# Performance work log

Hardware: AMD Instinct MI355X
Metric: run time of the kernel (lower is better)

The kernel has to match this reference:

```python
import jax, jax.numpy as jnp
import numpy as np

N_WORDS = 4096
N_HEADS = 512
EMB = 768          # input_size
HID = 1024         # hidden_size
DIST = 64          # dist_emb_size (forced by Conv1d(64, ...))
SENT_LEN = 64      # fixed sentence length -> static max padded length
PAIR_F = 2 * EMB + DIST  # 1600


def setup_inputs() -> dict:
    key = jax.random.key(0)
    ks = jax.random.split(key, 14)
    words = jax.random.normal(ks[0], (N_WORDS, EMB), dtype=jnp.float32)
    heads_ids = jax.random.randint(ks[1], (N_HEADS,), 0, N_WORDS, dtype=jnp.int64)
    sent_id = (jnp.arange(N_WORDS) // SENT_LEN).astype(jnp.int32)  # sorted, contiguous sentences
    s = 0.02
    return {
        "words": words,
        "heads_ids": heads_ids,
        "sent_id": sent_id,
        "emb_table": jax.random.normal(ks[2], (128, DIST), dtype=jnp.float32) * s,
        "W1": jax.random.normal(ks[3], (PAIR_F, HID), dtype=jnp.float32) * s,
        "b1": jnp.zeros((HID,), jnp.float32),
        "W2": jax.random.normal(ks[4], (HID, 256), dtype=jnp.float32) * s,
        "b2": jnp.zeros((256,), jnp.float32),
        "W3": jax.random.normal(ks[5], (256, DIST), dtype=jnp.float32) * s,
        "b3": jnp.zeros((DIST,), jnp.float32),
        "cw1": jax.random.normal(ks[6], (4, DIST, 3), dtype=jnp.float32) * s,  # Conv1d(64,4,3,1,1)
        "cb1": jnp.zeros((4,), jnp.float32),
        "cw2": jax.random.normal(ks[7], (2, 4, 3), dtype=jnp.float32) * s,    # Conv1d(4,2,3,1,1)
        "cb2": jnp.zeros((2,), jnp.float32),
    }


def _conv1d(x, w, b):
    # x: [N, C_in, L], w: [C_out, C_in, 3], padding=1, stride=1 (torch Conv1d semantics)
    y = jax.lax.conv_general_dilated(x, w, window_strides=(1,), padding=((1, 1),),
                                     dimension_numbers=("NCH", "OIH", "NCH"))
    return y + b[None, :, None]


def reference(words, heads_ids, sent_id, emb_table, W1, b1, W2, b2, W3, b3, cw1, cb1, cw2, cb2):
    n_words = words.shape[0]
    heads = heads_ids.astype(jnp.int32)
    H = heads.shape[0]

    # relative positions & distance-embedding ids, clamped to bucket 127 outside [-63, 63]
    rel = heads[:, None] - jnp.arange(n_words, dtype=jnp.int32)[None, :]      # [H, W]
    eid = rel + 63
    eid = jnp.where((eid < 0) | (eid > 126), 127, eid)

    # per-head sentence span (sent_id is sorted & contiguous)
    sh = sent_id[heads]
    starts = jnp.searchsorted(sent_id, sh, side="left")
    lengths = jnp.searchsorted(sent_id, sh, side="right") - starts            # [H]

    # padded ragged layout: row i holds words of head i's sentence, left-packed
    j = jnp.arange(SENT_LEN, dtype=jnp.int32)
    cols = starts[:, None] + j[None, :]                                       # [H, L]
    mask = j[None, :] < lengths[:, None]                                      # [H, L]
    cols_c = jnp.clip(cols, 0, n_words - 1)

    head_w = words[heads]                                                     # [H, E]
    col_w = words[cols_c]                                                     # [H, L, E]
    dist = emb_table[jnp.take_along_axis(eid, cols_c, axis=1)]                # [H, L, DIST]
    feat = jnp.concatenate(
        [jnp.broadcast_to(head_w[:, None, :], col_w.shape), col_w, dist], axis=-1)
    feat = jnp.where(mask[..., None], feat, jnp.zeros((), feat.dtype))        # zero padding rows (as torch)

    # FFNN (dropout is identity in eval mode)
    x = jax.nn.relu(feat @ W1 + b1)
    x = jax.nn.relu(x @ W2 + b2)
    x = x @ W3 + b3                                                           # [H, L, 64]

    # conv stack over the padded ragged axis
    x = _conv1d(x.transpose(0, 2, 1), cw1, cb1)
    x = _conv1d(x, cw2, cb2)
    res = x.transpose(0, 2, 1)                                                # [H, L, 2]

    # scatter back into [H, n_words, 2]; masked slots get out-of-range col -> dropped
    rows = jnp.broadcast_to(jnp.arange(H, dtype=jnp.int32)[:, None], mask.shape)
    cols_sc = jnp.where(mask, cols, n_words)
    scores = jnp.full((H, n_words, 2), -jnp.inf, dtype=words.dtype)
    scores = scores.at[rows, cols_sc].set(res, mode="drop")

    # eval-mode validity log-mask
    valid_starts = jnp.log((rel >= 0).astype(words.dtype))
    valid_ends = jnp.log((rel <= 0).astype(words.dtype))
    valid = jnp.stack([valid_starts, valid_ends], axis=2)
    return scores + valid
```

## Files before the change

kernel.cpp:

```cpp
#include <hip/hip_runtime.h>
#include <math.h>

#define NW   4096
#define NH   512
#define EMBD 768
#define HIDD 1024
#define DISTD 64
#define SLEN 64

#define NEG_BIG (-1.0e30f)

typedef __attribute__((ext_vector_type(8))) short short8;
typedef __attribute__((ext_vector_type(16))) float f32x16;
typedef __attribute__((ext_vector_type(4))) float f32x4;

#define MFMA32(a, b, c) __builtin_amdgcn_mfma_f32_32x32x16_bf16((a), (b), (c), 0, 0, 0)
#define MFMA16(a, b, c) __builtin_amdgcn_mfma_f32_16x16x32_bf16((a), (b), (c), 0, 0, 0)

__device__ __forceinline__ unsigned short f2bf(float f) {
    unsigned u = __float_as_uint(f);
    u += 0x7FFFu + ((u >> 16) & 1u);
    return (unsigned short)(u >> 16);
}
__device__ __forceinline__ float bf2f(unsigned short s) {
    return __uint_as_float(((unsigned)s) << 16);
}
__device__ __forceinline__ unsigned cvtpk(float lo, float hi) {
    unsigned r;
    asm("v_cvt_pk_bf16_f32 %0, %1, %2" : "=v"(r) : "v"(lo), "v"(hi));
    return r;
}
__device__ __forceinline__ short8 pack8(float f0, float f1, float f2, float f3,
                                        float f4, float f5, float f6, float f7) {
    union { unsigned u[4]; short8 s; } r;
    r.u[0] = cvtpk(f0, f1); r.u[1] = cvtpk(f2, f3);
    r.u[2] = cvtpk(f4, f5); r.u[3] = cvtpk(f6, f7);
    return r.s;
}

__device__ __forceinline__ void pack_b32_dev(long t, const float* __restrict__ src,
                                             int ld, int nb32, int KB,
                                             unsigned short* __restrict__ dst)
{
    int l = (int)(t & 63); long u = t >> 6;
    int nb = (int)(u % nb32); int kb = (int)(u / nb32);
    int row0 = kb * 16 + ((l >> 5) << 3);
    int col  = (nb << 5) + (l & 31);
    const float* s = src + (size_t)row0 * ld + col;
    short8 v;
#pragma unroll
    for (int j = 0; j < 8; ++j) v[j] = (short)f2bf(s[(size_t)j * ld]);
    *(short8*)(dst + (((size_t)nb * KB + kb) << 9) + l * 8) = v;
}

__device__ __forceinline__ void pack_b16_dev(long t, const float* __restrict__ src,
                                             int ld, int nb16, int KB,
                                             unsigned short* __restrict__ dst)
{
    int l = (int)(t & 63); long u = t >> 6;
    int nb = (int)(u % nb16); int kb = (int)(u / nb16);
    int row0 = kb * 32 + ((l >> 4) << 3);
    int col  = (nb << 4) + (l & 15);
    const float* s = src + (size_t)row0 * ld + col;
    short8 v;
#pragma unroll
    for (int j = 0; j < 8; ++j) v[j] = (short)f2bf(s[(size_t)j * ld]);
    *(short8*)(dst + (((size_t)nb * KB + kb) << 9) + l * 8) = v;
}

__device__ __forceinline__ void cvt8_dev(long i, const float* __restrict__ src,
                                         unsigned short* __restrict__ dst)
{
    const float* s = src + i * 8;
    short8 v;
#pragma unroll
    for (int j = 0; j < 8; ++j) v[j] = (short)f2bf(s[j]);
    *(short8*)(dst + i * 8) = v;
}

__global__ __launch_bounds__(256)
void prep_kernel(const float* __restrict__ words, const float* __restrict__ emb,
                 const float* __restrict__ W1, const float* __restrict__ W2,
                 const float* __restrict__ W3,
                 const int* __restrict__ heads, const int* __restrict__ sent_id,
                 unsigned short* __restrict__ wordsb, unsigned short* __restrict__ wpack,
                 unsigned short* __restrict__ embb,
                 unsigned short* __restrict__ W1pa, unsigned short* __restrict__ W1px,
                 unsigned short* __restrict__ W1pd,
                 unsigned short* __restrict__ W2p, unsigned short* __restrict__ W3p,
                 int* __restrict__ starts, int* __restrict__ lens)
{
    const int b = blockIdx.x, tid = threadIdx.x;
    if (b < 1536) {
        cvt8_dev((long)b * 256 + tid, words, wordsb);
    } else if (b < 3072) {
        long t = (long)(b - 1536) * 256 + tid;
        int r = (int)(t / 96), g = (int)(t % 96);
        const float* s = words + (size_t)r * EMBD + g * 8;
        short8 v;
#pragma unroll
        for (int j = 0; j < 8; ++j) v[j] = (short)f2bf(s[j]);
        int m = r >> 5, kb = g >> 1, lane = (r & 31) + 32 * (g & 1);
        *(short8*)(wpack + (((size_t)m * 48 + kb) << 9) + lane * 8) = v;
    } else if (b < 3076) {
        cvt8_dev((long)(b - 3072) * 256 + tid, emb, embb);
    } else if (b < 3460) {
        pack_b32_dev((long)(b - 3076) * 256 + tid, W1, HIDD, 32, 48, W1pa);
    } else if (b < 3844) {
        pack_b32_dev((long)(b - 3460) * 256 + tid, W1 + (size_t)768 * HIDD, HIDD, 32, 48, W1px);
    } else if (b < 3876) {
        pack_b32_dev((long)(b - 3844) * 256 + tid, W1 + (size_t)1536 * HIDD, HIDD, 32, 4, W1pd);
    } else if (b < 4004) {
        pack_b32_dev((long)(b - 3876) * 256 + tid, W2, 256, 8, 64, W2p);
    } else if (b < 4012) {
        pack_b16_dev((long)(b - 4004) * 256 + tid, W3, 64, 4, 8, W3p);
    } else {
        int h = (b - 4012) * 256 + tid;
        if (h < NH) {
            int head = heads[h];
            int s = sent_id[head];
            int lo = 0, hi = NW;
            while (lo < hi) { int mid = (lo + hi) >> 1; if (sent_id[mid] < s) lo = mid + 1; else hi = mid; }
            int start = lo;
            lo = 0; hi = NW;
            while (lo < hi) { int mid = (lo + hi) >> 1; if (sent_id[mid] <= s) lo = mid + 1; else hi = mid; }
            int len = lo - start;
            if (len > SLEN) len = SLEN;
            starts[h] = start;
            lens[h] = len;
        }
    }
}

__global__ __launch_bounds__(256, 4)
void gemms_kernel(const unsigned short* __restrict__ wordsb,
                  const unsigned short* __restrict__ wpack,
                  const unsigned short* __restrict__ embb,
                  const unsigned short* __restrict__ W1pa,
                  const unsigned short* __restrict__ W1px,
                  const unsigned short* __restrict__ W1pd,
                  const float* __restrict__ b1, const int* __restrict__ heads,
                  unsigned short* __restrict__ XwP, unsigned short* __restrict__ Hcb,
                  unsigned short* __restrict__ Dtb)
{
    const int b = blockIdx.x, tid = threadIdx.x;
    const int l = tid & 63, w = tid >> 6;

    if (b < 1024) {
        const int mB = b >> 3, nB = b & 7;
        const int cbg = nB * 4 + w;
        const unsigned short* ap = wpack + (((size_t)mB * 48) << 9) + l * 8;
        const unsigned short* bp = W1px + (((size_t)cbg * 48) << 9) + l * 8;
        f32x16 acc = {};
#pragma unroll
        for (int kk = 0; kk < 48; ++kk) {
            short8 a = *(const short8*)(ap + ((size_t)kk << 9));
            short8 bb = *(const short8*)(bp + ((size_t)kk << 9));
            acc = MFMA32(a, bb, acc);
        }
        const int col = cbg * 32 + (l & 31);
        const float bv = b1[col];
        const int kb2 = 2 * cbg + ((l & 31) >> 4);
        const int j = l & 7;
        const int lhalf = 32 * ((l >> 3) & 1);
        unsigned short* cp = XwP + (((size_t)mB * 64 + kb2) << 9) + j;
#pragma unroll
        for (int r = 0; r < 16; ++r) {
            int rr = (r & 3) + 8 * (r >> 2) + 4 * (l >> 5);
            cp[(rr + lhalf) * 8] = f2bf(acc[r] + bv);
        }
    } else if (b < 1152) {
        const int q = b - 1024;
        const int mB = q >> 3, nB = q & 7;
        const int cbg = nB * 4 + w;
        int row = heads[mB * 32 + (l & 31)];
        const unsigned short* ap = wordsb + (size_t)row * EMBD + ((l >> 5) << 3);
        const unsigned short* bp = W1pa + (((size_t)cbg * 48) << 9) + l * 8;
        f32x16 acc = {};
#pragma unroll
        for (int kk = 0; kk < 48; ++kk) {
            short8 a = *(const short8*)(ap + kk * 16);
            short8 bb = *(const short8*)(bp + ((size_t)kk << 9));
            acc = MFMA32(a, bb, acc);
        }
        const int col = cbg * 32 + (l & 31);
#pragma unroll
        for (int r = 0; r < 16; ++r) {
            int rr = mB * 32 + (r & 3) + 8 * (r >> 2) + 4 * (l >> 5);
            Hcb[(size_t)rr * HIDD + col] = f2bf(acc[r]);
        }
    } else {
        const int q = b - 1152;
        const int mB = q >> 3, nB = q & 7;
        const int cbg = nB * 4 + w;
        const unsigned short* ap = embb + (size_t)(mB * 32 + (l & 31)) * DISTD + ((l >> 5) << 3);
        const unsigned short* bp = W1pd + (((size_t)cbg * 4) << 9) + l * 8;
        f32x16 acc = {};
#pragma unroll
        for (int kk = 0; kk < 4; ++kk) {
            short8 a = *(const short8*)(ap + kk * 16);
            short8 bb = *(const short8*)(bp + ((size_t)kk << 9));
            acc = MFMA32(a, bb, acc);
        }
        const int col = cbg * 32 + (l & 31);
#pragma unroll
        for (int r = 0; r < 16; ++r) {
            int rr = mB * 32 + (r & 3) + 8 * (r >> 2) + 4 * (l >> 5);
            Dtb[(size_t)rr * HIDD + col] = f2bf(acc[r]);
        }
    }
}

__global__ __launch_bounds__(256)
void packd_kernel(const unsigned short* __restrict__ Dtb,
                  unsigned short* __restrict__ PDr)
{
    const int tid = threadIdx.x, l = tid & 63;
    const int c = blockIdx.x * 4 + (tid >> 6);
    const int s = c / 192, rem = c % 192;
    const int m = rem >> 6, kb = rem & 63;
    const int row = 126 - (s + 32 * m + (l & 31));
    const int koff = kb * 16 + ((l >> 5) << 3);
    short8 v = *(const short8*)(Dtb + (size_t)row * HIDD + koff);
    *(short8*)(PDr + ((size_t)c << 9) + l * 8) = v;
}

#define NT 32
__global__ __launch_bounds__(512)
void head_kernel(const unsigned short* __restrict__ XwP,
                 const unsigned short* __restrict__ Hcb,
                 const unsigned short* __restrict__ PDr,
                 const unsigned short* __restrict__ W2p,
                 const float* __restrict__ b2,
                 const unsigned short* __restrict__ W3p,
                 const float* __restrict__ b3,
                 const float* __restrict__ cw1, const float* __restrict__ cb1,
                 const float* __restrict__ cw2, const float* __restrict__ cb2,
                 const int* __restrict__ heads, const int* __restrict__ starts,
                 const int* __restrict__ lens,
                 float* __restrict__ out)
{
    __shared__ char smem[67584];
    unsigned short* Ast = (unsigned short*)smem;
    unsigned short* Bst = (unsigned short*)(smem + 16384);
    unsigned short* x2s = (unsigned short*)smem;
    float* x3s = (float*)smem;
    float* y1s = (float*)(smem + 35328);
    float* y2s = (float*)(smem + 37376);

    const int tid = threadIdx.x;
    const int l = tid & 63, w = tid >> 6;
    const int h0 = blockIdx.x * 2;

    const int head0 = heads[h0],  head1 = heads[h0 + 1];
    const int strt0 = starts[h0], strt1 = starts[h0 + 1];
    const int len0  = lens[h0],   len1  = lens[h0 + 1];

    const int kkA = w >> 2, rb = w & 3;
    const int hbA = rb >> 1;
    const int headA = hbA ? head1 : head0;
    const int strtA = hbA ? strt1 : strt0;
    const int q0A = 63 - (headA - strtA);
    const unsigned short* xwPp =
        XwP + (((size_t)((strtA >> 5) + (rb & 1)) * 64) << 9) + l * 8;
    const unsigned short* ddPp =
        PDr + (((size_t)((q0A & 31) * 3 + (q0A >> 5) + (rb & 1)) * 64) << 9) + l * 8;
    const unsigned short* hcp = Hcb + (size_t)(h0 + hbA) * HIDD + ((l >> 5) << 3);
    const int kkB = w >> 2, nbB0 = (w & 3) * 2;
    const int mb = w & 1, nq = w >> 1;

    f32x16 acc[2][2] = {};

    short8 rxw, rhc, rdd, rb0, rb1;

#define LOADT(t)                                                              \
    {                                                                         \
        const int kb_ = (t) * 2 + kkA;                                        \
        rxw = *(const short8*)(xwPp + ((size_t)kb_ << 9));                    \
        rdd = *(const short8*)(ddPp + ((size_t)kb_ << 9));                    \
        rhc = *(const short8*)(hcp + kb_ * 16);                               \
        const size_t c0_ = ((size_t)(nbB0 * 64 + (t) * 2 + kkB)) << 9;        \
        rb0 = *(const short8*)(W2p + c0_ + l * 8);                            \
        rb1 = *(const short8*)(W2p + c0_ + 32768 + l * 8);                    \
    }

#define WRITET(t)                                                             \
    {                                                                         \
        const int buf_ = (t) & 1;                                             \
        float f_[8];                                                          \
        _Pragma("unroll")                                                     \
        for (int j = 0; j < 8; ++j)                                           \
            f_[j] = fmaxf(bf2f((unsigned short)rxw[j])                        \
                        + bf2f((unsigned short)rhc[j])                        \
                        + bf2f((unsigned short)rdd[j]), 0.f);                 \
        short8 v_ = pack8(f_[0], f_[1], f_[2], f_[3], f_[4], f_[5], f_[6], f_[7]); \
        *(short8*)&Ast[buf_ * 4096 + (kkA * 4 + rb) * 512 + l * 8] = v_;      \
        *(short8*)&Bst[buf_ * 8192 + (kkB * 8 + nbB0) * 512 + l * 8] = rb0;   \
        *(short8*)&Bst[buf_ * 8192 + (kkB * 8 + nbB0 + 1) * 512 + l * 8] = rb1; \
    }

    LOADT(0);
    WRITET(0);
    LOADT(1);
    __syncthreads();

#pragma unroll 2
    for (int t = 0; t < NT; ++t) {
        const int buf = t & 1;
        short8 af0[2], af1[2], bf0[2], bf1[2];
#pragma unroll
        for (int k2 = 0; k2 < 2; ++k2) {
            af0[k2] = *(const short8*)&Ast[buf * 4096 + (k2 * 4 + mb * 2 + 0) * 512 + l * 8];
            af1[k2] = *(const short8*)&Ast[buf * 4096 + (k2 * 4 + mb * 2 + 1) * 512 + l * 8];
            bf0[k2] = *(const short8*)&Bst[buf * 8192 + (k2 * 8 + nq * 2 + 0) * 512 + l * 8];
            bf1[k2] = *(const short8*)&Bst[buf * 8192 + (k2 * 8 + nq * 2 + 1) * 512 + l * 8];
        }
        if (t + 1 < NT) WRITET(t + 1);
        if (t + 2 < NT) LOADT(t + 2);
        __builtin_amdgcn_s_setprio(1);
#pragma unroll
        for (int k2 = 0; k2 < 2; ++k2) {
            acc[0][0] = MFMA32(af0[k2], bf0[k2], acc[0][0]);
            acc[0][1] = MFMA32(af0[k2], bf1[k2], acc[0][1]);
            acc[1][0] = MFMA32(af1[k2], bf0[k2], acc[1][0]);
            acc[1][1] = MFMA32(af1[k2], bf1[k2], acc[1][1]);
        }
        __builtin_amdgcn_s_setprio(0);
        __syncthreads();
    }

#pragma unroll
    for (int i = 0; i < 2; ++i) {
#pragma unroll
        for (int n = 0; n < 2; ++n) {
            const int ct = nq * 64 + n * 32 + (l & 31);
            const float bv = b2[ct];
#pragma unroll
            for (int r = 0; r < 16; ++r) {
                const int rt = mb * 64 + i * 32 + (r & 3) + 8 * (r >> 2) + 4 * (l >> 5);
                const int hb = rt >> 6, rl = rt & 63;
                x2s[hb * 16896 + rl * 264 + ct] = f2bf(fmaxf(acc[i][n][r] + bv, 0.f));
            }
        }
    }
    __syncthreads();

    {
        const int hb = w >> 2, q = w & 3;
        const unsigned short* x2h = x2s + hb * 16896;
        f32x4 acc2[4] = {};
#pragma unroll
        for (int kk = 0; kk < 8; ++kk) {
            short8 bf = *(const short8*)(W3p + ((q * 8 + kk) << 9) + l * 8);
#pragma unroll
            for (int mi = 0; mi < 4; ++mi) {
                short8 af = *(const short8*)&x2h[(mi * 16 + (l & 15)) * 264 + kk * 32 + ((l >> 4) << 3)];
                acc2[mi] = MFMA16(af, bf, acc2[mi]);
            }
        }
        __syncthreads();
        float* x3h = x3s + hb * 4416;
        const int col = q * 16 + (l & 15);
        const float b3v = b3[col];
#pragma unroll
        for (int mi = 0; mi < 4; ++mi) {
#pragma unroll
            for (int r = 0; r < 4; ++r) {
                const int rowv = mi * 16 + (l >> 4) * 4 + r;
                x3h[rowv * 69 + col] = acc2[mi][r] + b3v;
            }
        }
    }
    __syncthreads();

    {
        const int hb3 = tid >> 8;
        const int co = (tid >> 6) & 3;
        const int ll = tid & 63;
        const float* x3h = x3s + hb3 * 4416;
        float s = cb1[co];
        const float* wb = cw1 + co * DISTD * 3;
        for (int ci = 0; ci < DISTD; ++ci) {
            float w0 = wb[ci * 3 + 0], w1 = wb[ci * 3 + 1], w2v = wb[ci * 3 + 2];
            float xm = (ll > 0) ? x3h[(ll - 1) * 69 + ci] : 0.f;
            float xc = x3h[ll * 69 + ci];
            float xp = (ll < 63) ? x3h[(ll + 1) * 69 + ci] : 0.f;
            s = fmaf(xm, w0, s);
            s = fmaf(xc, w1, s);
            s = fmaf(xp, w2v, s);
        }
        y1s[hb3 * 256 + co * 64 + ll] = s;
    }
    __syncthreads();

    if (tid < 256) {
        const int hb4 = tid >> 7;
        const int co = (tid >> 6) & 1;
        const int ll = tid & 63;
        const float* yh = y1s + hb4 * 256;
        const int head = hb4 ? head1 : head0;
        const int strt = hb4 ? strt1 : strt0;
        float s = cb2[co];
#pragma unroll
        for (int ci = 0; ci < 4; ++ci) {
            const float* wb = cw2 + (co * 4 + ci) * 3;
            const float* yr = yh + ci * 64;
            float xm = (ll > 0) ? yr[ll - 1] : 0.f;
            float xc = yr[ll];
            float xp = (ll < 63) ? yr[ll + 1] : 0.f;
            s = fmaf(xm, wb[0], s);
            s = fmaf(xc, wb[1], s);
            s = fmaf(xp, wb[2], s);
        }
        const int col = strt + ll;
        const int rel = head - col;
        const bool valid = (co == 0) ? (rel >= 0) : (rel <= 0);
        y2s[hb4 * 128 + ll * 2 + co] = valid ? s : NEG_BIG;
    }
    __syncthreads();

    {
        const int hb = tid >> 8;
        const int c8 = tid & 255;
        const int strt = hb ? strt1 : strt0;
        const int len  = hb ? len1  : len0;
        float* orow = out + ((size_t)(h0 + hb) * NW) * 2;
        const float* yh = y2s + hb * 128;
#pragma unroll
        for (int i = 0; i < 16; ++i) {
            const int col = i * 256 + c8;
            float2 v;
            if (col >= strt && col < strt + len) {
                v = *(const float2*)&yh[(col - strt) * 2];
            } else {
                v.x = NEG_BIG; v.y = NEG_BIG;
            }
            *(float2*)&orow[(size_t)col * 2] = v;
        }
    }
}

extern "C" void kernel_launch(void* const* d_in, const int* in_sizes, int n_in,
                              void* d_out, int out_size, void* d_ws, size_t ws_size,
                              hipStream_t stream)
{
    const float* words = (const float*)d_in[0];
    const int* heads   = (const int*)d_in[1];
    const int* sent_id = (const int*)d_in[2];
    const float* emb   = (const float*)d_in[3];
    const float* W1    = (const float*)d_in[4];
    const float* b1    = (const float*)d_in[5];
    const float* W2    = (const float*)d_in[6];
    const float* b2    = (const float*)d_in[7];
    const float* W3    = (const float*)d_in[8];
    const float* b3    = (const float*)d_in[9];
    const float* cw1   = (const float*)d_in[10];
    const float* cb1   = (const float*)d_in[11];
    const float* cw2   = (const float*)d_in[12];
    const float* cb2   = (const float*)d_in[13];
    float* out = (float*)d_out;

    char* wsb = (char*)d_ws;
    unsigned short* XwP  = (unsigned short*)(wsb + 0);
    unsigned short* Hcb  = (unsigned short*)(wsb + 8388608);
    unsigned short* Dtb  = (unsigned short*)(wsb + 9437184);
    unsigned short* W2p  = (unsigned short*)(wsb + 9699328);
    unsigned short* W3p  = (unsigned short*)(wsb + 10223616);
    unsigned short* PDr  = (unsigned short*)(wsb + 10256384);
    unsigned short* embb = (unsigned short*)(wsb + 16547840);
    int* starts          = (int*)(wsb + 16564224);
    int* lens            = (int*)(wsb + 16566272);
    char* ob = (char*)d_out;
    unsigned short* wordsb = (unsigned short*)(ob + 0);
    unsigned short* wpack  = (unsigned short*)(ob + 6291456);
    unsigned short* W1pa   = (unsigned short*)(ob + 12582912);
    unsigned short* W1px   = (unsigned short*)(ob + 14155776);
    unsigned short* W1pd   = (unsigned short*)(ob + 15728640);
    (void)ws_size; (void)in_sizes; (void)n_in; (void)out_size;

    prep_kernel<<<dim3(4014), dim3(256), 0, stream>>>(
        words, emb, W1, W2, W3, heads, sent_id,
        wordsb, wpack, embb, W1pa, W1px, W1pd, W2p, W3p, starts, lens);

    gemms_kernel<<<dim3(1184), dim3(256), 0, stream>>>(
        wordsb, wpack, embb, W1pa, W1px, W1pd, b1, heads, XwP, Hcb, Dtb);

    packd_kernel<<<dim3(1536), dim3(256), 0, stream>>>(Dtb, PDr);

    head_kernel<<<dim3(NH / 2), dim3(512), 0, stream>>>(
        XwP, Hcb, PDr, W2p, b2, W3p, b3, cw1, cb1, cw2, cb2,
        heads, starts, lens, out);
}
```

Measured before the change: 76.14 us.

## Drop row-major bf16 words copy, stage XwP stores via LDS, one head per block

The prep kernel no longer writes a row-major bf16 copy of words. The head-gather GEMM now reads rows directly from the MFMA-packed wpack layout. The XwP epilogue is transposed through a small LDS tile so each lane issues two 16-byte stores instead of 16 scattered 2-byte stores. The head kernel is restructured to process one head per 256-thread block with 512 blocks, halving LDS use to allow two blocks per CU, and each wave now computes a 32x128 tile with 4 accumulators. The trade-off is less reuse of W2 across heads, so W2 tiles are reloaded twice as often.

```diff
diff --git a/kernel.cpp b/kernel.cpp
--- a/kernel.cpp
+++ b/kernel.cpp
@@ -83,8 +83,7 @@
                  const float* __restrict__ W1, const float* __restrict__ W2,
                  const float* __restrict__ W3,
                  const int* __restrict__ heads, const int* __restrict__ sent_id,
-                 unsigned short* __restrict__ wordsb, unsigned short* __restrict__ wpack,
-                 unsigned short* __restrict__ embb,
+                 unsigned short* __restrict__ wpack, unsigned short* __restrict__ embb,
                  unsigned short* __restrict__ W1pa, unsigned short* __restrict__ W1px,
                  unsigned short* __restrict__ W1pd,
                  unsigned short* __restrict__ W2p, unsigned short* __restrict__ W3p,
@@ -92,9 +91,7 @@
 {
     const int b = blockIdx.x, tid = threadIdx.x;
     if (b < 1536) {
-        cvt8_dev((long)b * 256 + tid, words, wordsb);
-    } else if (b < 3072) {
-        long t = (long)(b - 1536) * 256 + tid;
+        long t = (long)b * 256 + tid;
         int r = (int)(t / 96), g = (int)(t % 96);
         const float* s = words + (size_t)r * EMBD + g * 8;
         short8 v;
@@ -102,20 +99,20 @@
         for (int j = 0; j < 8; ++j) v[j] = (short)f2bf(s[j]);
         int m = r >> 5, kb = g >> 1, lane = (r & 31) + 32 * (g & 1);
         *(short8*)(wpack + (((size_t)m * 48 + kb) << 9) + lane * 8) = v;
-    } else if (b < 3076) {
-        cvt8_dev((long)(b - 3072) * 256 + tid, emb, embb);
-    } else if (b < 3460) {
-        pack_b32_dev((long)(b - 3076) * 256 + tid, W1, HIDD, 32, 48, W1pa);
-    } else if (b < 3844) {
-        pack_b32_dev((long)(b - 3460) * 256 + tid, W1 + (size_t)768 * HIDD, HIDD, 32, 48, W1px);
-    } else if (b < 3876) {
-        pack_b32_dev((long)(b - 3844) * 256 + tid, W1 + (size_t)1536 * HIDD, HIDD, 32, 4, W1pd);
-    } else if (b < 4004) {
-        pack_b32_dev((long)(b - 3876) * 256 + tid, W2, 256, 8, 64, W2p);
-    } else if (b < 4012) {
-        pack_b16_dev((long)(b - 4004) * 256 + tid, W3, 64, 4, 8, W3p);
+    } else if (b < 1540) {
+        cvt8_dev((long)(b - 1536) * 256 + tid, emb, embb);
+    } else if (b < 1924) {
+        pack_b32_dev((long)(b - 1540) * 256 + tid, W1, HIDD, 32, 48, W1pa);
+    } else if (b < 2308) {
+        pack_b32_dev((long)(b - 1924) * 256 + tid, W1 + (size_t)768 * HIDD, HIDD, 32, 48, W1px);
+    } else if (b < 2340) {
+        pack_b32_dev((long)(b - 2308) * 256 + tid, W1 + (size_t)1536 * HIDD, HIDD, 32, 4, W1pd);
+    } else if (b < 2468) {
+        pack_b32_dev((long)(b - 2340) * 256 + tid, W2, 256, 8, 64, W2p);
+    } else if (b < 2476) {
+        pack_b16_dev((long)(b - 2468) * 256 + tid, W3, 64, 4, 8, W3p);
     } else {
-        int h = (b - 4012) * 256 + tid;
+        int h = (b - 2476) * 256 + tid;
         if (h < NH) {
             int head = heads[h];
             int s = sent_id[head];
@@ -133,8 +130,7 @@
 }
 
 __global__ __launch_bounds__(256, 4)
-void gemms_kernel(const unsigned short* __restrict__ wordsb,
-                  const unsigned short* __restrict__ wpack,
+void gemms_kernel(const unsigned short* __restrict__ wpack,
                   const unsigned short* __restrict__ embb,
                   const unsigned short* __restrict__ W1pa,
                   const unsigned short* __restrict__ W1px,
@@ -143,6 +139,8 @@
                   unsigned short* __restrict__ XwP, unsigned short* __restrict__ Hcb,
                   unsigned short* __restrict__ Dtb)
 {
+    __shared__ unsigned short tls[4][32 * 40];
+
     const int b = blockIdx.x, tid = threadIdx.x;
     const int l = tid & 63, w = tid >> 6;
 
@@ -160,26 +158,28 @@
         }
         const int col = cbg * 32 + (l & 31);
         const float bv = b1[col];
-        const int kb2 = 2 * cbg + ((l & 31) >> 4);
-        const int j = l & 7;
-        const int lhalf = 32 * ((l >> 3) & 1);
-        unsigned short* cp = XwP + (((size_t)mB * 64 + kb2) << 9) + j;
+        unsigned short* tw = tls[w];
 #pragma unroll
         for (int r = 0; r < 16; ++r) {
-            int rr = (r & 3) + 8 * (r >> 2) + 4 * (l >> 5);
-            cp[(rr + lhalf) * 8] = f2bf(acc[r] + bv);
-        }
+            int rowl = (r & 3) + 8 * (r >> 2) + 4 * (l >> 5);
+            tw[rowl * 40 + (l & 31)] = f2bf(acc[r] + bv);
+        }
+        short8 v0 = *(const short8*)&tw[(l & 31) * 40 + ((l >> 5) << 3)];
+        short8 v1 = *(const short8*)&tw[(l & 31) * 40 + 16 + ((l >> 5) << 3)];
+        *(short8*)(XwP + (((size_t)(mB * 64 + cbg * 2)) << 9) + l * 8) = v0;
+        *(short8*)(XwP + (((size_t)(mB * 64 + cbg * 2 + 1)) << 9) + l * 8) = v1;
     } else if (b < 1152) {
         const int q = b - 1024;
         const int mB = q >> 3, nB = q & 7;
         const int cbg = nB * 4 + w;
         int row = heads[mB * 32 + (l & 31)];
-        const unsigned short* ap = wordsb + (size_t)row * EMBD + ((l >> 5) << 3);
+        const unsigned short* ap = wpack + (((size_t)(row >> 5) * 48) << 9)
+                                 + ((row & 31) + 32 * (l >> 5)) * 8;
         const unsigned short* bp = W1pa + (((size_t)cbg * 48) << 9) + l * 8;
         f32x16 acc = {};
 #pragma unroll
         for (int kk = 0; kk < 48; ++kk) {
-            short8 a = *(const short8*)(ap + kk * 16);
+            short8 a = *(const short8*)(ap + ((size_t)kk << 9));
             short8 bb = *(const short8*)(bp + ((size_t)kk << 9));
             acc = MFMA32(a, bb, acc);
         }
@@ -226,7 +226,7 @@
 }
 
 #define NT 32
-__global__ __launch_bounds__(512)
+__global__ __launch_bounds__(256, 2)
 void head_kernel(const unsigned short* __restrict__ XwP,
                  const unsigned short* __restrict__ Hcb,
                  const unsigned short* __restrict__ PDr,
@@ -240,48 +240,48 @@
                  const int* __restrict__ lens,
                  float* __restrict__ out)
 {
-    __shared__ char smem[67584];
+    __shared__ char smem[40960];
     unsigned short* Ast = (unsigned short*)smem;
-    unsigned short* Bst = (unsigned short*)(smem + 16384);
+    unsigned short* Bst = (unsigned short*)(smem + 8192);
     unsigned short* x2s = (unsigned short*)smem;
     float* x3s = (float*)smem;
-    float* y1s = (float*)(smem + 35328);
-    float* y2s = (float*)(smem + 37376);
+    float* y1s = (float*)(smem + 17664);
+    float* y2s = (float*)(smem + 18688);
 
     const int tid = threadIdx.x;
     const int l = tid & 63, w = tid >> 6;
-    const int h0 = blockIdx.x * 2;
-
-    const int head0 = heads[h0],  head1 = heads[h0 + 1];
-    const int strt0 = starts[h0], strt1 = starts[h0 + 1];
-    const int len0  = lens[h0],   len1  = lens[h0 + 1];
-
-    const int kkA = w >> 2, rb = w & 3;
-    const int hbA = rb >> 1;
-    const int headA = hbA ? head1 : head0;
-    const int strtA = hbA ? strt1 : strt0;
-    const int q0A = 63 - (headA - strtA);
+    const int h = blockIdx.x;
+
+    const int head = heads[h];
+    const int strt = starts[h];
+    const int len  = lens[h];
+
+    const int kkA = w & 1, rb = w >> 1;
+    const int q0 = 63 - (head - strt);
     const unsigned short* xwPp =
-        XwP + (((size_t)((strtA >> 5) + (rb & 1)) * 64) << 9) + l * 8;
+        XwP + (((size_t)((strt >> 5) + rb) * 64) << 9) + l * 8;
     const unsigned short* ddPp =
-        PDr + (((size_t)((q0A & 31) * 3 + (q0A >> 5) + (rb & 1)) * 64) << 9) + l * 8;
-    const unsigned short* hcp = Hcb + (size_t)(h0 + hbA) * HIDD + ((l >> 5) << 3);
-    const int kkB = w >> 2, nbB0 = (w & 3) * 2;
-    const int mb = w & 1, nq = w >> 1;
-
-    f32x16 acc[2][2] = {};
-
-    short8 rxw, rhc, rdd, rb0, rb1;
+        PDr + (((size_t)((q0 & 31) * 3 + (q0 >> 5) + rb) * 64) << 9) + l * 8;
+    const unsigned short* hcp = Hcb + (size_t)h * HIDD + ((l >> 5) << 3);
+    const int nb0 = w * 2;
+    const int mbw = w & 1, nc = w >> 1;
+
+    f32x16 acc[4] = {};
+
+    short8 rxw, rhc, rdd, rb00, rb01, rb10, rb11;
 
 #define LOADT(t)                                                              \
     {                                                                         \
-        const int kb_ = (t) * 2 + kkA;                                        \
-        rxw = *(const short8*)(xwPp + ((size_t)kb_ << 9));                    \
-        rdd = *(const short8*)(ddPp + ((size_t)kb_ << 9));                    \
-        rhc = *(const short8*)(hcp + kb_ * 16);                               \
-        const size_t c0_ = ((size_t)(nbB0 * 64 + (t) * 2 + kkB)) << 9;        \
-        rb0 = *(const short8*)(W2p + c0_ + l * 8);                            \
-        rb1 = *(const short8*)(W2p + c0_ + 32768 + l * 8);                    \
+        const int kbA_ = (t) * 2 + kkA;                                       \
+        rxw = *(const short8*)(xwPp + ((size_t)kbA_ << 9));                   \
+        rdd = *(const short8*)(ddPp + ((size_t)kbA_ << 9));                   \
+        rhc = *(const short8*)(hcp + kbA_ * 16);                              \
+        const size_t c00_ = ((size_t)(nb0 * 64 + (t) * 2)) << 9;              \
+        const size_t c01_ = ((size_t)((nb0 + 1) * 64 + (t) * 2)) << 9;        \
+        rb00 = *(const short8*)(W2p + c00_ + l * 8);                          \
+        rb01 = *(const short8*)(W2p + c01_ + l * 8);                          \
+        rb10 = *(const short8*)(W2p + c00_ + 512 + l * 8);                    \
+        rb11 = *(const short8*)(W2p + c01_ + 512 + l * 8);                    \
     }
 
 #define WRITET(t)                                                             \
@@ -294,9 +294,11 @@
                         + bf2f((unsigned short)rhc[j])                        \
                         + bf2f((unsigned short)rdd[j]), 0.f);                 \
         short8 v_ = pack8(f_[0], f_[1], f_[2], f_[3], f_[4], f_[5], f_[6], f_[7]); \
-        *(short8*)&Ast[buf_ * 4096 + (kkA * 4 + rb) * 512 + l * 8] = v_;      \
-        *(short8*)&Bst[buf_ * 8192 + (kkB * 8 + nbB0) * 512 + l * 8] = rb0;   \
-        *(short8*)&Bst[buf_ * 8192 + (kkB * 8 + nbB0 + 1) * 512 + l * 8] = rb1; \
+        *(short8*)&Ast[buf_ * 2048 + (kkA * 2 + rb) * 512 + l * 8] = v_;      \
+        *(short8*)&Bst[buf_ * 8192 + (nb0) * 512 + l * 8] = rb00;             \
+        *(short8*)&Bst[buf_ * 8192 + (nb0 + 1) * 512 + l * 8] = rb01;         \
+        *(short8*)&Bst[buf_ * 8192 + (8 + nb0) * 512 + l * 8] = rb10;         \
+        *(short8*)&Bst[buf_ * 8192 + (8 + nb0 + 1) * 512 + l * 8] = rb11;     \
     }
 
     LOADT(0);
@@ -307,104 +309,89 @@
 #pragma unroll 2
     for (int t = 0; t < NT; ++t) {
         const int buf = t & 1;
-        short8 af0[2], af1[2], bf0[2], bf1[2];
+        short8 af[2], bf[2][4];
 #pragma unroll
         for (int k2 = 0; k2 < 2; ++k2) {
-            af0[k2] = *(const short8*)&Ast[buf * 4096 + (k2 * 4 + mb * 2 + 0) * 512 + l * 8];
-            af1[k2] = *(const short8*)&Ast[buf * 4096 + (k2 * 4 + mb * 2 + 1) * 512 + l * 8];
-            bf0[k2] = *(const short8*)&Bst[buf * 8192 + (k2 * 8 + nq * 2 + 0) * 512 + l * 8];
-            bf1[k2] = *(const short8*)&Bst[buf * 8192 + (k2 * 8 + nq * 2 + 1) * 512 + l * 8];
+            af[k2] = *(const short8*)&Ast[buf * 2048 + (k2 * 2 + mbw) * 512 + l * 8];
+#pragma unroll
+            for (int n = 0; n < 4; ++n)
+                bf[k2][n] = *(const short8*)&Bst[buf * 8192 + (k2 * 8 + nc * 4 + n) * 512 + l * 8];
         }
         if (t + 1 < NT) WRITET(t + 1);
         if (t + 2 < NT) LOADT(t + 2);
         __builtin_amdgcn_s_setprio(1);
 #pragma unroll
-        for (int k2 = 0; k2 < 2; ++k2) {
-            acc[0][0] = MFMA32(af0[k2], bf0[k2], acc[0][0]);
-            acc[0][1] = MFMA32(af0[k2], bf1[k2], acc[0][1]);
-            acc[1][0] = MFMA32(af1[k2], bf0[k2], acc[1][0]);
-            acc[1][1] = MFMA32(af1[k2], bf1[k2], acc[1][1]);
-        }
+        for (int k2 = 0; k2 < 2; ++k2)
+#pragma unroll
+            for (int n = 0; n < 4; ++n)
+                acc[n] = MFMA32(af[k2], bf[k2][n], acc[n]);
         __builtin_amdgcn_s_setprio(0);
         __syncthreads();
     }
 
 #pragma unroll
-    for (int i = 0; i < 2; ++i) {
-#pragma unroll
-        for (int n = 0; n < 2; ++n) {
-            const int ct = nq * 64 + n * 32 + (l & 31);
-            const float bv = b2[ct];
-#pragma unroll
-            for (int r = 0; r < 16; ++r) {
-                const int rt = mb * 64 + i * 32 + (r & 3) + 8 * (r >> 2) + 4 * (l >> 5);
-                const int hb = rt >> 6, rl = rt & 63;
-                x2s[hb * 16896 + rl * 264 + ct] = f2bf(fmaxf(acc[i][n][r] + bv, 0.f));
+    for (int n = 0; n < 4; ++n) {
+        const int ct = nc * 128 + n * 32 + (l & 31);
+        const float bv = b2[ct];
+#pragma unroll
+        for (int r = 0; r < 16; ++r) {
+            const int rt = mbw * 32 + (r & 3) + 8 * (r >> 2) + 4 * (l >> 5);
+            x2s[rt * 264 + ct] = f2bf(fmaxf(acc[n][r] + bv, 0.f));
+        }
+    }
+    __syncthreads();
+
+    {
+        f32x4 acc2[4] = {};
+#pragma unroll
+        for (int kk = 0; kk < 8; ++kk) {
+            short8 bfr = *(const short8*)(W3p + ((w * 8 + kk) << 9) + l * 8);
+#pragma unroll
+            for (int mi = 0; mi < 4; ++mi) {
+                short8 afr = *(const short8*)&x2s[(mi * 16 + (l & 15)) * 264 + kk * 32 + ((l >> 4) << 3)];
+                acc2[mi] = MFMA16(afr, bfr, acc2[mi]);
             }
         }
-    }
-    __syncthreads();
-
-    {
-        const int hb = w >> 2, q = w & 3;
-        const unsigned short* x2h = x2s + hb * 16896;
-        f32x4 acc2[4] = {};
-#pragma unroll
-        for (int kk = 0; kk < 8; ++kk) {
-            short8 bf = *(const short8*)(W3p + ((q * 8 + kk) << 9) + l * 8);
-#pragma unroll
-            for (int mi = 0; mi < 4; ++mi) {
-                short8 af = *(const short8*)&x2h[(mi * 16 + (l & 15)) * 264 + kk * 32 + ((l >> 4) << 3)];
-                acc2[mi] = MFMA16(af, bf, acc2[mi]);
-            }
-        }
         __syncthreads();
-        float* x3h = x3s + hb * 4416;
-        const int col = q * 16 + (l & 15);
+        const int col = w * 16 + (l & 15);
         const float b3v = b3[col];
 #pragma unroll
         for (int mi = 0; mi < 4; ++mi) {
 #pragma unroll
             for (int r = 0; r < 4; ++r) {
                 const int rowv = mi * 16 + (l >> 4) * 4 + r;
-                x3h[rowv * 69 + col] = acc2[mi][r] + b3v;
+                x3s[rowv * 69 + col] = acc2[mi][r] + b3v;
             }
         }
     }
     __syncthreads();
 
     {
-        const int hb3 = tid >> 8;
-        const int co = (tid >> 6) & 3;
+        const int co = tid >> 6;
         const int ll = tid & 63;
-        const float* x3h = x3s + hb3 * 4416;
         float s = cb1[co];
         const float* wb = cw1 + co * DISTD * 3;
         for (int ci = 0; ci < DISTD; ++ci) {
             float w0 = wb[ci * 3 + 0], w1 = wb[ci * 3 + 1], w2v = wb[ci * 3 + 2];
-            float xm = (ll > 0) ? x3h[(ll - 1) * 69 + ci] : 0.f;
-            float xc = x3h[ll * 69 + ci];
-            float xp = (ll < 63) ? x3h[(ll + 1) * 69 + ci] : 0.f;
+            float xm = (ll > 0) ? x3s[(ll - 1) * 69 + ci] : 0.f;
+            float xc = x3s[ll * 69 + ci];
+            float xp = (ll < 63) ? x3s[(ll + 1) * 69 + ci] : 0.f;
             s = fmaf(xm, w0, s);
             s = fmaf(xc, w1, s);
             s = fmaf(xp, w2v, s);
         }
-        y1s[hb3 * 256 + co * 64 + ll] = s;
+        y1s[co * 64 + ll] = s;
     }
     __syncthreads();
 
-    if (tid < 256) {
-        const int hb4 = tid >> 7;
-        const int co = (tid >> 6) & 1;
+    if (tid < 128) {
+        const int co = tid >> 6;
         const int ll = tid & 63;
-        const float* yh = y1s + hb4 * 256;
-        const int head = hb4 ? head1 : head0;
-        const int strt = hb4 ? strt1 : strt0;
         float s = cb2[co];
 #pragma unroll
         for (int ci = 0; ci < 4; ++ci) {
             const float* wb = cw2 + (co * 4 + ci) * 3;
-            const float* yr = yh + ci * 64;
+            const float* yr = y1s + ci * 64;
             float xm = (ll > 0) ? yr[ll - 1] : 0.f;
             float xc = yr[ll];
             float xp = (ll < 63) ? yr[ll + 1] : 0.f;
@@ -415,23 +402,18 @@
         const int col = strt + ll;
         const int rel = head - col;
         const bool valid = (co == 0) ? (rel >= 0) : (rel <= 0);
-        y2s[hb4 * 128 + ll * 2 + co] = valid ? s : NEG_BIG;
+        y2s[ll * 2 + co] = valid ? s : NEG_BIG;
     }
     __syncthreads();
 
     {
-        const int hb = tid >> 8;
-        const int c8 = tid & 255;
-        const int strt = hb ? strt1 : strt0;
-        const int len  = hb ? len1  : len0;
-        float* orow = out + ((size_t)(h0 + hb) * NW) * 2;
-        const float* yh = y2s + hb * 128;
+        float* orow = out + ((size_t)h * NW) * 2;
 #pragma unroll
         for (int i = 0; i < 16; ++i) {
-            const int col = i * 256 + c8;
+            const int col = i * 256 + tid;
             float2 v;
             if (col >= strt && col < strt + len) {
-                v = *(const float2*)&yh[(col - strt) * 2];
+                v = *(const float2*)&y2s[(col - strt) * 2];
             } else {
                 v.x = NEG_BIG; v.y = NEG_BIG;
             }
@@ -471,23 +453,22 @@
     int* starts          = (int*)(wsb + 16564224);
     int* lens            = (int*)(wsb + 16566272);
     char* ob = (char*)d_out;
-    unsigned short* wordsb = (unsigned short*)(ob + 0);
-    unsigned short* wpack  = (unsigned short*)(ob + 6291456);
-    unsigned short* W1pa   = (unsigned short*)(ob + 12582912);
-    unsigned short* W1px   = (unsigned short*)(ob + 14155776);
-    unsigned short* W1pd   = (unsigned short*)(ob + 15728640);
+    unsigned short* wpack  = (unsigned short*)(ob + 0);
+    unsigned short* W1pa   = (unsigned short*)(ob + 6291456);
+    unsigned short* W1px   = (unsigned short*)(ob + 7864320);
+    unsigned short* W1pd   = (unsigned short*)(ob + 9437184);
     (void)ws_size; (void)in_sizes; (void)n_in; (void)out_size;
 
-    prep_kernel<<<dim3(4014), dim3(256), 0, stream>>>(
+    prep_kernel<<<dim3(2478), dim3(256), 0, stream>>>(
         words, emb, W1, W2, W3, heads, sent_id,
-        wordsb, wpack, embb, W1pa, W1px, W1pd, W2p, W3p, starts, lens);
+        wpack, embb, W1pa, W1px, W1pd, W2p, W3p, starts, lens);
 
     gemms_kernel<<<dim3(1184), dim3(256), 0, stream>>>(
-        wordsb, wpack, embb, W1pa, W1px, W1pd, b1, heads, XwP, Hcb, Dtb);
+        wpack, embb, W1pa, W1px, W1pd, b1, heads, XwP, Hcb, Dtb);
 
     packd_kernel<<<dim3(1536), dim3(256), 0, stream>>>(Dtb, PDr);
 
-    head_kernel<<<dim3(NH / 2), dim3(512), 0, stream>>>(
+    head_kernel<<<dim3(NH), dim3(256), 0, stream>>>(
         XwP, Hcb, PDr, W2p, b2, W3p, b3, cw1, cb1, cw2, cb2,
         heads, starts, lens, out);
 }
```

Result: slower. 82.03 us (+7.7%).

## Drop row-major bf16 words copy, widen gemm tiles, LDS-staged output, deeper pipeline

Applied to the files above, without the earlier changes.

The prep kernel no longer writes a separate row-major bf16 copy of words; the head-row GEMM instead reads gathered rows straight from the MFMA-packed layout. The words×W1 GEMM now computes two 32-row tiles per block so each B fragment is reused, halving the grid. Its output is staged through LDS to produce coalesced 16-byte stores instead of scattered 2-byte stores. The head kernel's K loop gets double register staging so global loads run two tiles ahead. Together these cut prep traffic and store inefficiency, at the cost of extra LDS, more registers and fewer blocks.

```diff
diff --git a/kernel.cpp b/kernel.cpp
--- a/kernel.cpp
+++ b/kernel.cpp
@@ -83,8 +83,7 @@
                  const float* __restrict__ W1, const float* __restrict__ W2,
                  const float* __restrict__ W3,
                  const int* __restrict__ heads, const int* __restrict__ sent_id,
-                 unsigned short* __restrict__ wordsb, unsigned short* __restrict__ wpack,
-                 unsigned short* __restrict__ embb,
+                 unsigned short* __restrict__ wpack, unsigned short* __restrict__ embb,
                  unsigned short* __restrict__ W1pa, unsigned short* __restrict__ W1px,
                  unsigned short* __restrict__ W1pd,
                  unsigned short* __restrict__ W2p, unsigned short* __restrict__ W3p,
@@ -92,9 +91,7 @@
 {
     const int b = blockIdx.x, tid = threadIdx.x;
     if (b < 1536) {
-        cvt8_dev((long)b * 256 + tid, words, wordsb);
-    } else if (b < 3072) {
-        long t = (long)(b - 1536) * 256 + tid;
+        long t = (long)b * 256 + tid;
         int r = (int)(t / 96), g = (int)(t % 96);
         const float* s = words + (size_t)r * EMBD + g * 8;
         short8 v;
@@ -102,20 +99,20 @@
         for (int j = 0; j < 8; ++j) v[j] = (short)f2bf(s[j]);
         int m = r >> 5, kb = g >> 1, lane = (r & 31) + 32 * (g & 1);
         *(short8*)(wpack + (((size_t)m * 48 + kb) << 9) + lane * 8) = v;
-    } else if (b < 3076) {
-        cvt8_dev((long)(b - 3072) * 256 + tid, emb, embb);
-    } else if (b < 3460) {
-        pack_b32_dev((long)(b - 3076) * 256 + tid, W1, HIDD, 32, 48, W1pa);
-    } else if (b < 3844) {
-        pack_b32_dev((long)(b - 3460) * 256 + tid, W1 + (size_t)768 * HIDD, HIDD, 32, 48, W1px);
-    } else if (b < 3876) {
-        pack_b32_dev((long)(b - 3844) * 256 + tid, W1 + (size_t)1536 * HIDD, HIDD, 32, 4, W1pd);
-    } else if (b < 4004) {
-        pack_b32_dev((long)(b - 3876) * 256 + tid, W2, 256, 8, 64, W2p);
-    } else if (b < 4012) {
-        pack_b16_dev((long)(b - 4004) * 256 + tid, W3, 64, 4, 8, W3p);
+    } else if (b < 1540) {
+        cvt8_dev((long)(b - 1536) * 256 + tid, emb, embb);
+    } else if (b < 1924) {
+        pack_b32_dev((long)(b - 1540) * 256 + tid, W1, HIDD, 32, 48, W1pa);
+    } else if (b < 2308) {
+        pack_b32_dev((long)(b - 1924) * 256 + tid, W1 + (size_t)768 * HIDD, HIDD, 32, 48, W1px);
+    } else if (b < 2340) {
+        pack_b32_dev((long)(b - 2308) * 256 + tid, W1 + (size_t)1536 * HIDD, HIDD, 32, 4, W1pd);
+    } else if (b < 2468) {
+        pack_b32_dev((long)(b - 2340) * 256 + tid, W2, 256, 8, 64, W2p);
+    } else if (b < 2476) {
+        pack_b16_dev((long)(b - 2468) * 256 + tid, W3, 64, 4, 8, W3p);
     } else {
-        int h = (b - 4012) * 256 + tid;
+        int h = (b - 2476) * 256 + tid;
         if (h < NH) {
             int head = heads[h];
             int s = sent_id[head];
@@ -133,8 +130,7 @@
 }
 
 __global__ __launch_bounds__(256, 4)
-void gemms_kernel(const unsigned short* __restrict__ wordsb,
-                  const unsigned short* __restrict__ wpack,
+void gemms_kernel(const unsigned short* __restrict__ wpack,
                   const unsigned short* __restrict__ embb,
                   const unsigned short* __restrict__ W1pa,
                   const unsigned short* __restrict__ W1px,
@@ -143,14 +139,53 @@
                   unsigned short* __restrict__ XwP, unsigned short* __restrict__ Hcb,
                   unsigned short* __restrict__ Dtb)
 {
+    __shared__ unsigned short tls[4][2][32 * 40];
+
     const int b = blockIdx.x, tid = threadIdx.x;
     const int l = tid & 63, w = tid >> 6;
 
-    if (b < 1024) {
-        const int mB = b >> 3, nB = b & 7;
+    if (b < 512) {
+        const int mB2 = b >> 3, nB = b & 7;
         const int cbg = nB * 4 + w;
-        const unsigned short* ap = wpack + (((size_t)mB * 48) << 9) + l * 8;
-        const unsigned short* bp = W1px + (((size_t)cbg * 48) << 9) + l * 8;
+        const unsigned short* ap0 = wpack + (((size_t)(mB2 * 2 + 0) * 48) << 9) + l * 8;
+        const unsigned short* ap1 = wpack + (((size_t)(mB2 * 2 + 1) * 48) << 9) + l * 8;
+        const unsigned short* bp  = W1px + (((size_t)cbg * 48) << 9) + l * 8;
+        f32x16 acc0 = {}, acc1 = {};
+#pragma unroll
+        for (int kk = 0; kk < 48; ++kk) {
+            short8 a0 = *(const short8*)(ap0 + ((size_t)kk << 9));
+            short8 a1 = *(const short8*)(ap1 + ((size_t)kk << 9));
+            short8 bb = *(const short8*)(bp + ((size_t)kk << 9));
+            acc0 = MFMA32(a0, bb, acc0);
+            acc1 = MFMA32(a1, bb, acc1);
+        }
+        const float bv = b1[cbg * 32 + (l & 31)];
+        unsigned short* tw0 = tls[w][0];
+        unsigned short* tw1 = tls[w][1];
+#pragma unroll
+        for (int r = 0; r < 16; ++r) {
+            int rowl = (r & 3) + 8 * (r >> 2) + 4 * (l >> 5);
+            tw0[rowl * 40 + (l & 31)] = f2bf(acc0[r] + bv);
+            tw1[rowl * 40 + (l & 31)] = f2bf(acc1[r] + bv);
+        }
+        short8 v00 = *(const short8*)&tw0[(l & 31) * 40 + ((l >> 5) << 3)];
+        short8 v01 = *(const short8*)&tw0[(l & 31) * 40 + 16 + ((l >> 5) << 3)];
+        short8 v10 = *(const short8*)&tw1[(l & 31) * 40 + ((l >> 5) << 3)];
+        short8 v11 = *(const short8*)&tw1[(l & 31) * 40 + 16 + ((l >> 5) << 3)];
+        const size_t c0 = ((size_t)((mB2 * 2 + 0) * 64 + cbg * 2)) << 9;
+        const size_t c1 = ((size_t)((mB2 * 2 + 1) * 64 + cbg * 2)) << 9;
+        *(short8*)(XwP + c0 + l * 8) = v00;
+        *(short8*)(XwP + c0 + 512 + l * 8) = v01;
+        *(short8*)(XwP + c1 + l * 8) = v10;
+        *(short8*)(XwP + c1 + 512 + l * 8) = v11;
+    } else if (b < 640) {
+        const int q = b - 512;
+        const int mB = q >> 3, nB = q & 7;
+        const int cbg = nB * 4 + w;
+        int row = heads[mB * 32 + (l & 31)];
+        const unsigned short* ap = wpack + (((size_t)(row >> 5) * 48) << 9)
+                                 + ((row & 31) + 32 * (l >> 5)) * 8;
+        const unsigned short* bp = W1pa + (((size_t)cbg * 48) << 9) + l * 8;
         f32x16 acc = {};
 #pragma unroll
         for (int kk = 0; kk < 48; ++kk) {
@@ -159,38 +194,13 @@
             acc = MFMA32(a, bb, acc);
         }
         const int col = cbg * 32 + (l & 31);
-        const float bv = b1[col];
-        const int kb2 = 2 * cbg + ((l & 31) >> 4);
-        const int j = l & 7;
-        const int lhalf = 32 * ((l >> 3) & 1);
-        unsigned short* cp = XwP + (((size_t)mB * 64 + kb2) << 9) + j;
-#pragma unroll
-        for (int r = 0; r < 16; ++r) {
-            int rr = (r & 3) + 8 * (r >> 2) + 4 * (l >> 5);
-            cp[(rr + lhalf) * 8] = f2bf(acc[r] + bv);
-        }
-    } else if (b < 1152) {
-        const int q = b - 1024;
-        const int mB = q >> 3, nB = q & 7;
-        const int cbg = nB * 4 + w;
-        int row = heads[mB * 32 + (l & 31)];
-        const unsigned short* ap = wordsb + (size_t)row * EMBD + ((l >> 5) << 3);
-        const unsigned short* bp = W1pa + (((size_t)cbg * 48) << 9) + l * 8;
-        f32x16 acc = {};
-#pragma unroll
-        for (int kk = 0; kk < 48; ++kk) {
-            short8 a = *(const short8*)(ap + kk * 16);
-            short8 bb = *(const short8*)(bp + ((size_t)kk << 9));
-            acc = MFMA32(a, bb, acc);
-        }
-        const int col = cbg * 32 + (l & 31);
 #pragma unroll
         for (int r = 0; r < 16; ++r) {
             int rr = mB * 32 + (r & 3) + 8 * (r >> 2) + 4 * (l >> 5);
             Hcb[(size_t)rr * HIDD + col] = f2bf(acc[r]);
         }
     } else {
-        const int q = b - 1152;
+        const int q = b - 640;
         const int mB = q >> 3, nB = q & 7;
         const int cbg = nB * 4 + w;
         const unsigned short* ap = embb + (size_t)(mB * 32 + (l & 31)) * DISTD + ((l >> 5) << 3);
@@ -271,61 +281,70 @@
 
     f32x16 acc[2][2] = {};
 
-    short8 rxw, rhc, rdd, rb0, rb1;
-
-#define LOADT(t)                                                              \
+    short8 xwS0, hcS0, ddS0, bS0a, bS0b;
+    short8 xwS1, hcS1, ddS1, bS1a, bS1b;
+
+#define LOADT(t, RXW, RHC, RDD, RB0, RB1)                                     \
     {                                                                         \
         const int kb_ = (t) * 2 + kkA;                                        \
-        rxw = *(const short8*)(xwPp + ((size_t)kb_ << 9));                    \
-        rdd = *(const short8*)(ddPp + ((size_t)kb_ << 9));                    \
-        rhc = *(const short8*)(hcp + kb_ * 16);                               \
+        RXW = *(const short8*)(xwPp + ((size_t)kb_ << 9));                    \
+        RDD = *(const short8*)(ddPp + ((size_t)kb_ << 9));                    \
+        RHC = *(const short8*)(hcp + kb_ * 16);                               \
         const size_t c0_ = ((size_t)(nbB0 * 64 + (t) * 2 + kkB)) << 9;        \
-        rb0 = *(const short8*)(W2p + c0_ + l * 8);                            \
-        rb1 = *(const short8*)(W2p + c0_ + 32768 + l * 8);                    \
-    }
-
-#define WRITET(t)                                                             \
+        RB0 = *(const short8*)(W2p + c0_ + l * 8);                            \
+        RB1 = *(const short8*)(W2p + c0_ + 32768 + l * 8);                    \
+    }
+
+#define WRITET(t, RXW, RHC, RDD, RB0, RB1)                                    \
     {                                                                         \
         const int buf_ = (t) & 1;                                             \
         float f_[8];                                                          \
         _Pragma("unroll")                                                     \
         for (int j = 0; j < 8; ++j)                                           \
-            f_[j] = fmaxf(bf2f((unsigned short)rxw[j])                        \
-                        + bf2f((unsigned short)rhc[j])                        \
-                        + bf2f((unsigned short)rdd[j]), 0.f);                 \
+            f_[j] = fmaxf(bf2f((unsigned short)RXW[j])                        \
+                        + bf2f((unsigned short)RHC[j])                        \
+                        + bf2f((unsigned short)RDD[j]), 0.f);                 \
         short8 v_ = pack8(f_[0], f_[1], f_[2], f_[3], f_[4], f_[5], f_[6], f_[7]); \
         *(short8*)&Ast[buf_ * 4096 + (kkA * 4 + rb) * 512 + l * 8] = v_;      \
-        *(short8*)&Bst[buf_ * 8192 + (kkB * 8 + nbB0) * 512 + l * 8] = rb0;   \
-        *(short8*)&Bst[buf_ * 8192 + (kkB * 8 + nbB0 + 1) * 512 + l * 8] = rb1; \
-    }
-
-    LOADT(0);
-    WRITET(0);
-    LOADT(1);
+        *(short8*)&Bst[buf_ * 8192 + (kkB * 8 + nbB0) * 512 + l * 8] = RB0;   \
+        *(short8*)&Bst[buf_ * 8192 + (kkB * 8 + nbB0 + 1) * 512 + l * 8] = RB1; \
+    }
+
+#define FRAGS_MFMA(buf_)                                                      \
+    {                                                                         \
+        short8 af0[2], af1[2], bf0[2], bf1[2];                                \
+        _Pragma("unroll")                                                     \
+        for (int k2 = 0; k2 < 2; ++k2) {                                      \
+            af0[k2] = *(const short8*)&Ast[(buf_) * 4096 + (k2 * 4 + mb * 2 + 0) * 512 + l * 8]; \
+            af1[k2] = *(const short8*)&Ast[(buf_) * 4096 + (k2 * 4 + mb * 2 + 1) * 512 + l * 8]; \
+            bf0[k2] = *(const short8*)&Bst[(buf_) * 8192 + (k2 * 8 + nq * 2 + 0) * 512 + l * 8]; \
+            bf1[k2] = *(const short8*)&Bst[(buf_) * 8192 + (k2 * 8 + nq * 2 + 1) * 512 + l * 8]; \
+        }                                                                     \
+        __builtin_amdgcn_s_setprio(1);                                        \
+        _Pragma("unroll")                                                     \
+        for (int k2 = 0; k2 < 2; ++k2) {                                      \
+            acc[0][0] = MFMA32(af0[k2], bf0[k2], acc[0][0]);                  \
+            acc[0][1] = MFMA32(af0[k2], bf1[k2], acc[0][1]);                  \
+            acc[1][0] = MFMA32(af1[k2], bf0[k2], acc[1][0]);                  \
+            acc[1][1] = MFMA32(af1[k2], bf1[k2], acc[1][1]);                  \
+        }                                                                     \
+        __builtin_amdgcn_s_setprio(0);                                        \
+    }
+
+    LOADT(0, xwS0, hcS0, ddS0, bS0a, bS0b);
+    LOADT(1, xwS1, hcS1, ddS1, bS1a, bS1b);
+    WRITET(0, xwS0, hcS0, ddS0, bS0a, bS0b);
+    LOADT(2, xwS0, hcS0, ddS0, bS0a, bS0b);
     __syncthreads();
 
-#pragma unroll 2
-    for (int t = 0; t < NT; ++t) {
-        const int buf = t & 1;
-        short8 af0[2], af1[2], bf0[2], bf1[2];
-#pragma unroll
-        for (int k2 = 0; k2 < 2; ++k2) {
-            af0[k2] = *(const short8*)&Ast[buf * 4096 + (k2 * 4 + mb * 2 + 0) * 512 + l * 8];
-            af1[k2] = *(const short8*)&Ast[buf * 4096 + (k2 * 4 + mb * 2 + 1) * 512 + l * 8];
-            bf0[k2] = *(const short8*)&Bst[buf * 8192 + (k2 * 8 + nq * 2 + 0) * 512 + l * 8];
-            bf1[k2] = *(const short8*)&Bst[buf * 8192 + (k2 * 8 + nq * 2 + 1) * 512 + l * 8];
-        }
-        if (t + 1 < NT) WRITET(t + 1);
-        if (t + 2 < NT) LOADT(t + 2);
-        __builtin_amdgcn_s_setprio(1);
-#pragma unroll
-        for (int k2 = 0; k2 < 2; ++k2) {
-            acc[0][0] = MFMA32(af0[k2], bf0[k2], acc[0][0]);
-            acc[0][1] = MFMA32(af0[k2], bf1[k2], acc[0][1]);
-            acc[1][0] = MFMA32(af1[k2], bf0[k2], acc[1][0]);
-            acc[1][1] = MFMA32(af1[k2], bf1[k2], acc[1][1]);
-        }
-        __builtin_amdgcn_s_setprio(0);
+    for (int t = 0; t < NT; t += 2) {
+        if (t + 1 < NT) WRITET(t + 1, xwS1, hcS1, ddS1, bS1a, bS1b);
+        if (t + 3 < NT) LOADT(t + 3, xwS1, hcS1, ddS1, bS1a, bS1b);
+        FRAGS_MFMA(0);
+        __syncthreads();
+        if (t + 2 < NT) WRITET(t + 2, xwS0, hcS0, ddS0, bS0a, bS0b);
+        if (t + 4 < NT) LOADT(t + 4, xwS0, hcS0, ddS0, bS0a, bS0b);
+        FRAGS_MFMA(1);
         __syncthreads();
     }
 
@@ -471,19 +490,18 @@
     int* starts          = (int*)(wsb + 16564224);
     int* lens            = (int*)(wsb + 16566272);
     char* ob = (char*)d_out;
-    unsigned short* wordsb = (unsigned short*)(ob + 0);
-    unsigned short* wpack  = (unsigned short*)(ob + 6291456);
-    unsigned short* W1pa   = (unsigned short*)(ob + 12582912);
-    unsigned short* W1px   = (unsigned short*)(ob + 14155776);
-    unsigned short* W1pd   = (unsigned short*)(ob + 15728640);
+    unsigned short* wpack  = (unsigned short*)(ob + 0);
+    unsigned short* W1pa   = (unsigned short*)(ob + 6291456);
+    unsigned short* W1px   = (unsigned short*)(ob + 7864320);
+    unsigned short* W1pd   = (unsigned short*)(ob + 9437184);
     (void)ws_size; (void)in_sizes; (void)n_in; (void)out_size;
 
-    prep_kernel<<<dim3(4014), dim3(256), 0, stream>>>(
+    prep_kernel<<<dim3(2478), dim3(256), 0, stream>>>(
         words, emb, W1, W2, W3, heads, sent_id,
-        wordsb, wpack, embb, W1pa, W1px, W1pd, W2p, W3p, starts, lens);
-
-    gemms_kernel<<<dim3(1184), dim3(256), 0, stream>>>(
-        wordsb, wpack, embb, W1pa, W1px, W1pd, b1, heads, XwP, Hcb, Dtb);
+        wpack, embb, W1pa, W1px, W1pd, W2p, W3p, starts, lens);
+
+    gemms_kernel<<<dim3(672), dim3(256), 0, stream>>>(
+        wpack, embb, W1pa, W1px, W1pd, b1, heads, XwP, Hcb, Dtb);
 
     packd_kernel<<<dim3(1536), dim3(256), 0, stream>>>(Dtb, PDr);
 
```

Result: slower. 79.97 us (+5.0%).
